# Kernel tuning notes

Hardware: AMD Instinct MI355X
Metric: run time of the kernel (lower is better)

Reference implementation:

```python
import jax, jax.numpy as jnp
import numpy as np

N, E, KS, DIM = 6890, 41340, 5, 2
K = KS * KS  # 25 spline kernel buckets


def spline_conv(x, edge_index, pseudo, weight, root, bias):
    """Degree-1 open B-spline conv (SplineGCN), mean aggregation + root + bias.
    x: [N, Fin], weight: [K, Fin, Fout], root: [Fin, Fout], bias: [Fout]."""
    row, col = edge_index[0], edge_index[1]  # target, source
    pos = pseudo * (KS - 1)                   # [E, 2] in [0, KS-1]
    i0 = jnp.clip(jnp.floor(pos), 0, KS - 2).astype(jnp.int32)  # [E, 2]
    frac = pos - i0                           # [E, 2]
    # 4 nonzero basis products per edge (2 per dim)
    off = jnp.array([[0, 0], [1, 0], [0, 1], [1, 1]], dtype=jnp.int32)  # [4, 2]
    b_dim = jnp.stack([1.0 - frac, frac], axis=-1)  # [E, 2, 2] (dim, which-knot)
    w = b_dim[:, 0, off[:, 0]] * b_dim[:, 1, off[:, 1]]       # [E, 4]
    idx = (i0[:, None, 0] + off[None, :, 0]) + KS * (i0[:, None, 1] + off[None, :, 1])  # [E, 4]
    # transform all nodes by all K kernels once: [N, K, Fout]
    xw = jnp.einsum('ni,kio->nko', x, weight)
    g = xw[col[:, None], idx]                 # [E, 4, Fout] gather
    msg = jnp.einsum('es,eso->eo', w, g)      # [E, Fout]
    agg = jax.ops.segment_sum(msg, row, num_segments=N)
    deg = jax.ops.segment_sum(jnp.ones((E,), x.dtype), row, num_segments=N)
    agg = agg / jnp.maximum(deg, 1.0)[:, None]
    return agg + x @ root + bias


def setup_inputs() -> dict:
    key = jax.random.key(0)
    ks = jax.random.split(key, 20)
    def gl(k, shape):  # glorot-ish
        fan = shape[-2] if len(shape) > 1 else shape[-1]
        return jax.random.normal(k, shape, jnp.float32) / np.sqrt(fan)
    inp = {
        'x': jax.random.normal(ks[0], (N, 544), jnp.float32),
        'edge_index': jax.random.randint(ks[1], (2, E), 0, N),
        'pseudo': jax.random.uniform(ks[2], (E, DIM), jnp.float32),
        'W_lin': gl(ks[3], (544, 16)), 'b_lin': jnp.zeros((16,), jnp.float32),
        'w1': gl(ks[4], (K, 16, 32)),  'r1': gl(ks[5], (16, 32)),  'bi1': jnp.zeros((32,), jnp.float32),
        'w2': gl(ks[6], (K, 32, 64)),  'r2': gl(ks[7], (32, 64)),  'bi2': jnp.zeros((64,), jnp.float32),
        'w3': gl(ks[8], (K, 64, 128)), 'r3': gl(ks[9], (64, 128)), 'bi3': jnp.zeros((128,), jnp.float32),
        'W1': gl(ks[10], (128, 256)), 'b1': jnp.zeros((256,), jnp.float32),
        'W2': gl(ks[11], (256, 6890)), 'b2': jnp.zeros((6890,), jnp.float32),
    }
    return inp


def reference(x, edge_index, pseudo, W_lin, b_lin, w1, r1, bi1, w2, r2, bi2, w3, r3, bi3, W1, b1, W2, b2):
    h = jax.nn.elu(x @ W_lin + b_lin)
    h = jax.nn.elu(spline_conv(h, edge_index, pseudo, w1, r1, bi1))
    h = jax.nn.elu(spline_conv(h, edge_index, pseudo, w2, r2, bi2))
    h = jax.nn.elu(spline_conv(h, edge_index, pseudo, w3, r3, bi3))
    h = jax.nn.elu(h @ W1 + b1)
    # dropout is identity in eval mode
    logits = h @ W2 + b2
    return jax.nn.log_softmax(logits, axis=-1)
```

## Files before the change

### kernel.cpp

```cpp
#include <hip/hip_runtime.h>
#include <hip/hip_bf16.h>

#define NND 6890
#define NED 41340

typedef __bf16 bf16x8 __attribute__((ext_vector_type(8)));
typedef float f32x4 __attribute__((ext_vector_type(4)));
typedef unsigned short u16x4 __attribute__((ext_vector_type(4)));

__device__ inline unsigned short f32_bf16(float f) {
  unsigned int u = __float_as_uint(f);
  unsigned int r = (u + 0x7FFFu + ((u >> 16) & 1u)) >> 16;
  return (unsigned short)r;
}
__device__ inline void split2(float v, unsigned short& hi, unsigned short& lo) {
  unsigned short h = f32_bf16(v);
  float hf = __uint_as_float((unsigned int)h << 16);
  hi = h;
  lo = f32_bf16(v - hf);
}
__device__ inline float elu_f(float v) { return v > 0.f ? v : (expf(v) - 1.f); }

__device__ __forceinline__ void gload_lds16(const void* g, void* l) {
  __builtin_amdgcn_global_load_lds((const __attribute__((address_space(1))) void*)g,
                                   (__attribute__((address_space(3))) void*)l, 16, 0, 0);
}

__global__ void edge_prep_kernel(const int* __restrict__ erow, const float* __restrict__ pseudo,
                                 float* __restrict__ ew, int* __restrict__ ek,
                                 int* __restrict__ deg, int E) {
  int e = blockIdx.x * blockDim.x + threadIdx.x;
  if (e >= E) return;
  float p0 = pseudo[2 * e + 0] * 4.0f;
  float p1 = pseudo[2 * e + 1] * 4.0f;
  int i0 = (int)floorf(p0); i0 = i0 < 0 ? 0 : (i0 > 3 ? 3 : i0);
  int i1 = (int)floorf(p1); i1 = i1 < 0 ? 0 : (i1 > 3 ? 3 : i1);
  float f0 = p0 - (float)i0, f1 = p1 - (float)i1;
  ew[4 * e + 0] = (1.f - f0) * (1.f - f1);
  ew[4 * e + 1] = f0 * (1.f - f1);
  ew[4 * e + 2] = (1.f - f0) * f1;
  ew[4 * e + 3] = f0 * f1;
  int b = i0 + 5 * i1;
  ek[4 * e + 0] = b; ek[4 * e + 1] = b + 1; ek[4 * e + 2] = b + 5; ek[4 * e + 3] = b + 6;
  atomicAdd(&deg[erow[e]], 1);
}

__global__ void scan_kernel(const int* __restrict__ deg, int* __restrict__ rowptr,
                            int* __restrict__ cursor, float* __restrict__ deginv, int n) {
  __shared__ int part[1024];
  int t = threadIdx.x;
  int CH = (n + 1023) >> 10;
  int base = t * CH;
  int s = 0;
  for (int j = 0; j < CH; ++j) { int i = base + j; if (i < n) s += deg[i]; }
  part[t] = s;
  __syncthreads();
  for (int off = 1; off < 1024; off <<= 1) {
    int v = (t >= off) ? part[t - off] : 0;
    __syncthreads();
    part[t] += v;
    __syncthreads();
  }
  int run = (t == 0) ? 0 : part[t - 1];
  for (int j = 0; j < CH; ++j) {
    int i = base + j;
    if (i < n) {
      rowptr[i] = run; cursor[i] = run;
      int d = deg[i];
      deginv[i] = 1.0f / fmaxf((float)d, 1.0f);
      run += d;
    }
  }
  if (t == 1023) rowptr[n] = part[1023];
}

__global__ void csr_fill_kernel(const int* __restrict__ erow, int* __restrict__ cursor,
                                int* __restrict__ csr, int E) {
  int e = blockIdx.x * blockDim.x + threadIdx.x;
  if (e >= E) return;
  int slot = atomicAdd(&cursor[erow[e]], 1);
  csr[slot] = e;
}

__global__ void prep_all_kernel(const float* __restrict__ W_lin, const float* __restrict__ w1,
                                const float* __restrict__ r1, const float* __restrict__ w2,
                                const float* __restrict__ r2, const float* __restrict__ w3,
                                const float* __restrict__ r3, const float* __restrict__ W1,
                                const float* __restrict__ x, const float* __restrict__ W2,
                                unsigned short* __restrict__ Th, unsigned short* __restrict__ Tl,
                                unsigned short* __restrict__ xh, unsigned short* __restrict__ xl,
                                unsigned short* __restrict__ W2t) {
  int b = blockIdx.x;
  int tid = threadIdx.x;
  if (b < 323) {
    const int tstart[9] = {0, 17, 30, 31, 81, 83, 283, 291, 323};
    const int jK[8]    = {544, 400, 16, 800, 32, 1600, 64, 128};
    const int jF[8]    = {16, 32, 32, 64, 64, 128, 128, 256};
    const int jldt[8]  = {544, 416, 416, 832, 832, 1664, 1664, 128};
    const int jkoff[8] = {0, 0, 400, 0, 800, 0, 1600, 0};
    const int jdst[8]  = {0, 8704, 8704, 22016, 22016, 75264, 75264, 288256};
    int job = 0;
    while (job < 7 && b >= tstart[job + 1]) ++job;
    int t = b - tstart[job];
    int fxc = (jF[job] + 31) >> 5;
    int kt = t / fxc, ft = t % fxc;
    const float* src;
    switch (job) {
      case 0: src = W_lin; break;
      case 1: src = w1; break;
      case 2: src = r1; break;
      case 3: src = w2; break;
      case 4: src = r2; break;
      case 5: src = w3; break;
      case 6: src = r3; break;
      default: src = W1; break;
    }
    int K = jK[job], F = jF[job], ldt = jldt[job], koff = jkoff[job];
    unsigned short* th = Th + jdst[job];
    unsigned short* tl = Tl + jdst[job];
    int k0 = kt * 32, c0 = ft * 32;
    __shared__ float tbuf[32][33];
    int tx = tid & 31, ty = tid >> 5;
    for (int j = ty; j < 32; j += 8) {
      int gk = k0 + j, gc = c0 + tx;
      tbuf[j][tx] = (gk < K && gc < F) ? src[(size_t)gk * F + gc] : 0.f;
    }
    __syncthreads();
    for (int j = ty; j < 32; j += 8) {
      int gc = c0 + j, gk = k0 + tx;
      if (gc < F && gk < K) {
        unsigned short h, lo2;
        split2(tbuf[tx][j], h, lo2);
        th[(size_t)gc * ldt + koff + gk] = h;
        tl[(size_t)gc * ldt + koff + gk] = lo2;
      }
    }
  } else if (b < 3984) {
    int i = (b - 323) * 256 + tid;
    if (i < NND * 136) {
      f32x4 v = *(const f32x4*)(x + 4 * (size_t)i);
      u16x4 h, l;
#pragma unroll
      for (int j = 0; j < 4; ++j) {
        unsigned short hh, ll;
        split2(v[j], hh, ll);
        h[j] = hh; l[j] = ll;
      }
      *(u16x4*)(xh + 4 * (size_t)i) = h;
      *(u16x4*)(xl + 4 * (size_t)i) = l;
    }
  } else {
    int t = b - 3984;
    int c0 = (t % 216) * 32, k0 = (t / 216) * 32;
    __shared__ float tb2[32][33];
    int tx = tid & 31, ty = tid >> 5;
    for (int j = ty; j < 32; j += 8) {
      int gk = k0 + j, gc = c0 + tx;
      tb2[j][tx] = (gk < 256 && gc < NND) ? W2[(size_t)gk * NND + gc] : 0.f;
    }
    __syncthreads();
    for (int j = ty; j < 32; j += 8) {
      int gc = c0 + j, gk = k0 + tx;
      if (gc < NND && gk < 256) W2t[(size_t)gc * 256 + gk] = f32_bf16(tb2[tx][j]);
    }
  }
}

__global__ void b_build_kernel(const float* __restrict__ x, const int* __restrict__ ecol,
                               const float* __restrict__ ew4, const int* __restrict__ ek4,
                               const int* __restrict__ rowptr, const int* __restrict__ csr,
                               const float* __restrict__ deginv,
                               unsigned short* __restrict__ Bh, unsigned short* __restrict__ Bl,
                               int Fin) {
  extern __shared__ float lds[];
  int r = blockIdx.x;
  int T = blockDim.x;
  int tid = threadIdx.x;
  int nb = 25 * Fin;
  int j = tid / Fin;
  int i = tid - j * Fin;
  float* plane = lds + j * nb;
  for (int t = tid; t < 4 * nb; t += T) lds[t] = 0.f;
  __syncthreads();
  int p0 = rowptr[r], p1 = rowptr[r + 1];
  for (int p = p0 + j; p < p1; p += 4) {
    int e = csr[p];
    int c = ecol[e];
    float xv = x[(size_t)c * Fin + i];
    f32x4 wv = *(const f32x4*)(ew4 + 4 * e);
    int4 kv = *(const int4*)(ek4 + 4 * e);
    plane[kv.x * Fin + i] += wv[0] * xv;
    plane[kv.y * Fin + i] += wv[1] * xv;
    plane[kv.z * Fin + i] += wv[2] * xv;
    plane[kv.w * Fin + i] += wv[3] * xv;
  }
  __syncthreads();
  float dinv = deginv[r];
  int tot = nb + Fin;
  for (int t = tid; t < tot; t += T) {
    float v;
    if (t < nb)
      v = (lds[t] + lds[nb + t] + lds[2 * nb + t] + lds[3 * nb + t]) * dinv;
    else
      v = x[(size_t)r * Fin + (t - nb)];
    unsigned short h, l;
    split2(v, h, l);
    Bh[(size_t)r * tot + t] = h;
    Bl[(size_t)r * tot + t] = l;
  }
}

template <int BN>
__global__ __launch_bounds__(256) void gemm_x3_partial_kernel(
    const unsigned short* __restrict__ Ah, const unsigned short* __restrict__ Al,
    const unsigned short* __restrict__ Wh, const unsigned short* __restrict__ Wl,
    float* __restrict__ P, int M, int Kd, int F, int KS) {
  constexpr int AE = 64 * 32;
  constexpr int WE = BN * 32;
  __shared__ __align__(16) unsigned short lds[2][2 * AE + 2 * WE];
  int tid = threadIdx.x;
  int wave = tid >> 6, lane = tid & 63;
  int g = lane >> 4, r = lane & 15;
  int row0 = blockIdx.y * 64;
  int col0 = blockIdx.x * BN;
  int z = blockIdx.z;
  int nt = Kd >> 5;
  int ta = z * nt / KS, tb = (z + 1) * nt / KS;

  auto STAGE = [&](int buf, int kb) {
    {
      int rr = tid >> 2, pos = tid & 3;
      int c = (pos - rr) & 3;
      int gra = row0 + rr; if (gra >= M) gra = M - 1;
      size_t so = (size_t)gra * Kd + kb + c * 8;
      gload_lds16(Ah + so, &lds[buf][wave * 512]);
      gload_lds16(Al + so, &lds[buf][AE + wave * 512]);
    }
#pragma unroll
    for (int it = 0; it < (4 * BN + 255) / 256; ++it) {
      int idx = it * 256 + tid;
      if (idx < 4 * BN) {
        int rr = idx >> 2, pos = idx & 3;
        int c = (pos - rr) & 3;
        size_t so = (size_t)(col0 + rr) * Kd + kb + c * 8;
        gload_lds16(Wh + so, &lds[buf][2 * AE + (it * 256 + wave * 64) * 8]);
        gload_lds16(Wl + so, &lds[buf][2 * AE + WE + (it * 256 + wave * 64) * 8]);
      }
    }
  };

  constexpr int NF = BN / 16;
  f32x4 acc[NF];
#pragma unroll
  for (int n = 0; n < NF; ++n)
#pragma unroll
    for (int q = 0; q < 4; ++q) acc[n][q] = 0.f;

  int n = tb - ta;
  int rA = wave * 16 + r;
  int aoff = rA * 32 + ((g + rA) & 3) * 8;

  STAGE(0, ta * 32);
  __syncthreads();
  for (int tt = 0; tt < n; ++tt) {
    int buf = tt & 1;
    if (tt + 1 < n) STAGE(buf ^ 1, (ta + tt + 1) * 32);
    bf16x8 fah = *(const bf16x8*)&lds[buf][aoff];
    bf16x8 fal = *(const bf16x8*)&lds[buf][AE + aoff];
#pragma unroll
    for (int nn = 0; nn < NF; ++nn) {
      int rW = nn * 16 + r;
      int woff = rW * 32 + ((g + rW) & 3) * 8;
      bf16x8 fbh = *(const bf16x8*)&lds[buf][2 * AE + woff];
      bf16x8 fbl = *(const bf16x8*)&lds[buf][2 * AE + WE + woff];
      acc[nn] = __builtin_amdgcn_mfma_f32_16x16x32_bf16(fah, fbh, acc[nn], 0, 0, 0);
      acc[nn] = __builtin_amdgcn_mfma_f32_16x16x32_bf16(fal, fbh, acc[nn], 0, 0, 0);
      acc[nn] = __builtin_amdgcn_mfma_f32_16x16x32_bf16(fah, fbl, acc[nn], 0, 0, 0);
    }
    __syncthreads();
  }
#pragma unroll
  for (int nn = 0; nn < NF; ++nn) {
    int gc = col0 + nn * 16 + r;
#pragma unroll
    for (int q = 0; q < 4; ++q) {
      int gr = row0 + wave * 16 + g * 4 + q;
      if (gr < M) P[((size_t)z * M + gr) * F + gc] = acc[nn][q];
    }
  }
}

__global__ __launch_bounds__(256) void combine_elu_kernel(
    const float* __restrict__ P, const float* __restrict__ bias,
    float* __restrict__ outF, unsigned short* __restrict__ outB,
    unsigned short* __restrict__ outH, unsigned short* __restrict__ outL,
    int M, int F, int KS) {
  int i4 = blockIdx.x * 256 + threadIdx.x;
  int fv = F >> 2;
  int total = M * fv;
  if (i4 >= total) return;
  int gr = i4 / fv, c4 = (i4 - gr * fv) * 4;
  f32x4 s = {0.f, 0.f, 0.f, 0.f};
  for (int z = 0; z < KS; ++z)
    s += *(const f32x4*)(P + ((size_t)z * M + gr) * F + c4);
  f32x4 bv = *(const f32x4*)(bias + c4);
#pragma unroll
  for (int j = 0; j < 4; ++j) s[j] = elu_f(s[j] + bv[j]);
  if (outH) {
    u16x4 h, l;
#pragma unroll
    for (int j = 0; j < 4; ++j) {
      unsigned short hh, ll;
      split2(s[j], hh, ll);
      h[j] = hh; l[j] = ll;
    }
    *(u16x4*)(outH + (size_t)gr * F + c4) = h;
    *(u16x4*)(outL + (size_t)gr * F + c4) = l;
  } else if (outB) {
    u16x4 o;
#pragma unroll
    for (int j = 0; j < 4; ++j) o[j] = f32_bf16(s[j]);
    *(u16x4*)(outB + (size_t)gr * F + c4) = o;
  } else {
    *(f32x4*)(outF + (size_t)gr * F + c4) = s;
  }
}

template <int MODE>
__global__ __launch_bounds__(256) void gemm_final_kernel(
    const unsigned short* __restrict__ A, const unsigned short* __restrict__ Bt,
    const float* __restrict__ bias, const float* __restrict__ lse,
    float* __restrict__ outp, int M, int N) {
  __shared__ __align__(16) unsigned short lds[2][2][4096];
  int tid = threadIdx.x;
  int w = tid >> 6, l = tid & 63;
  int row0 = blockIdx.y * 128, col0 = blockIdx.x * 128;

  auto STAGE = [&](int buf, int kb) {
#pragma unroll
    for (int it = 0; it < 2; ++it) {
      int idx = it * 256 + tid;
      int rr = idx >> 2, pos = idx & 3;
      int c = (pos - rr) & 3;
      int gra = row0 + rr; if (gra >= M) gra = M - 1;
      int grb = col0 + rr; if (grb >= N) grb = N - 1;
      gload_lds16(A + (size_t)gra * 256 + kb + c * 8, &lds[buf][0][(it * 256 + w * 64) * 8]);
      gload_lds16(Bt + (size_t)grb * 256 + kb + c * 8, &lds[buf][1][(it * 256 + w * 64) * 8]);
    }
  };

  int wm = w >> 1, wn = w & 1;
  int g = l >> 4, r = l & 15;

  f32x4 acc[4][4];
#pragma unroll
  for (int mi = 0; mi < 4; ++mi)
#pragma unroll
    for (int ni = 0; ni < 4; ++ni)
#pragma unroll
      for (int q = 0; q < 4; ++q) acc[mi][ni][q] = 0.f;

  STAGE(0, 0);
  __syncthreads();
#pragma unroll
  for (int ks = 0; ks < 8; ++ks) {
    int buf = ks & 1;
    if (ks < 7) STAGE(buf ^ 1, (ks + 1) * 32);
    bf16x8 fa[4], fb[4];
#pragma unroll
    for (int mi = 0; mi < 4; ++mi) {
      int rA = wm * 64 + mi * 16 + r;
      fa[mi] = *(const bf16x8*)&lds[buf][0][rA * 32 + ((g + rA) & 3) * 8];
    }
#pragma unroll
    for (int ni = 0; ni < 4; ++ni) {
      int rB = wn * 64 + ni * 16 + r;
      fb[ni] = *(const bf16x8*)&lds[buf][1][rB * 32 + ((g + rB) & 3) * 8];
    }
#pragma unroll
    for (int mi = 0; mi < 4; ++mi)
#pragma unroll
      for (int ni = 0; ni < 4; ++ni)
        acc[mi][ni] = __builtin_amdgcn_mfma_f32_16x16x32_bf16(fb[ni], fa[mi], acc[mi][ni], 0, 0, 0);
    __syncthreads();
  }

  if (MODE == 0) {
    float bb[4][4];
#pragma unroll
    for (int ni = 0; ni < 4; ++ni) {
      int gc0 = col0 + wn * 64 + ni * 16 + g * 4;
#pragma unroll
      for (int q = 0; q < 4; ++q)
        bb[ni][q] = (gc0 + q < N) ? bias[gc0 + q] : 0.f;
    }
#pragma unroll
    for (int mi = 0; mi < 4; ++mi) {
      int gr = row0 + wm * 64 + mi * 16 + r;
      float vv[4][4];
      float mloc = -3e38f;
#pragma unroll
      for (int ni = 0; ni < 4; ++ni) {
        int gc0 = col0 + wn * 64 + ni * 16 + g * 4;
#pragma unroll
        for (int q = 0; q < 4; ++q) {
          float v = (gc0 + q < N) ? (acc[mi][ni][q] + bb[ni][q]) : -3e38f;
          vv[ni][q] = v;
          mloc = fmaxf(mloc, v);
        }
      }
      float sloc = 0.f;
#pragma unroll
      for (int ni = 0; ni < 4; ++ni) {
        int gc0 = col0 + wn * 64 + ni * 16 + g * 4;
#pragma unroll
        for (int q = 0; q < 4; ++q)
          if (gc0 + q < N) sloc += __expf(vv[ni][q] - mloc);
      }
#pragma unroll
      for (int off = 16; off < 64; off <<= 1) {
        float mo = __shfl_xor(mloc, off);
        float so = __shfl_xor(sloc, off);
        float mn = fmaxf(mloc, mo);
        sloc = sloc * __expf(mloc - mn) + so * __expf(mo - mn);
        mloc = mn;
      }
      if (g == 0 && gr < M) {
        int hb = blockIdx.x * 2 + wn;
        *(float2*)(outp + 2 * ((size_t)hb * M + gr)) = make_float2(mloc, sloc);
      }
    }
  } else {
    float* LBUF = (float*)&lds[0][0][0];
#pragma unroll
    for (int p = 0; p < 2; ++p) {
      __syncthreads();
#pragma unroll
      for (int mh = 0; mh < 2; ++mh) {
        int mi = 2 * p + mh;
        int lr = wm * 32 + mh * 16 + r;
#pragma unroll
        for (int ni = 0; ni < 4; ++ni) {
          int ch = wn * 16 + ni * 4 + g;
          int u = (ch + lr) & 31;
          *(f32x4*)(LBUF + lr * 128 + u * 4) = acc[mi][ni];
        }
      }
      __syncthreads();
#pragma unroll
      for (int t = 0; t < 8; ++t) {
        int unit = t * 256 + tid;
        int lr = unit >> 5, ch = unit & 31;
        int gr = row0 + (lr >> 5) * 64 + p * 32 + ((lr >> 4) & 1) * 16 + (lr & 15);
        if (gr >= M) continue;
        int u = (ch + lr) & 31;
        f32x4 v = *(const f32x4*)(LBUF + lr * 128 + u * 4);
        float L = lse[gr];
        int gc0 = col0 + ch * 4;
        if (gc0 + 4 <= N) {
          f32x4 bv = *(const f32x4*)(bias + gc0);
#pragma unroll
          for (int q = 0; q < 4; ++q) v[q] = v[q] + bv[q] - L;
          *(f32x4*)(outp + (size_t)gr * N + gc0) = v;
        } else {
#pragma unroll
          for (int q = 0; q < 4; ++q)
            if (gc0 + q < N) outp[(size_t)gr * N + gc0 + q] = v[q] + bias[gc0 + q] - L;
        }
      }
    }
  }
}

__global__ __launch_bounds__(256) void lse_kernel(const float* __restrict__ stats,
                                                  float* __restrict__ lse, int M, int NH) {
  int row = blockIdx.x * 256 + threadIdx.x;
  if (row >= M) return;
  float m = -3e38f, s = 0.f;
  for (int hb = 0; hb < NH; ++hb) {
    float2 v = *(const float2*)(stats + 2 * ((size_t)hb * M + row));
    float mn = fmaxf(m, v.x);
    s = s * __expf(m - mn) + v.y * __expf(v.x - mn);
    m = mn;
  }
  lse[row] = m + logf(s);
}

extern "C" void kernel_launch(void* const* d_in, const int* in_sizes, int n_in,
                              void* d_out, int out_size, void* d_ws, size_t ws_size,
                              hipStream_t stream) {
  const int N = NND, E = NED;
  const float* x      = (const float*)d_in[0];
  const int*   ei     = (const int*)d_in[1];
  const float* pseudo = (const float*)d_in[2];
  const float* W_lin  = (const float*)d_in[3];
  const float* b_lin  = (const float*)d_in[4];
  const float* w1  = (const float*)d_in[5];
  const float* r1  = (const float*)d_in[6];
  const float* bi1 = (const float*)d_in[7];
  const float* w2  = (const float*)d_in[8];
  const float* r2  = (const float*)d_in[9];
  const float* bi2 = (const float*)d_in[10];
  const float* w3  = (const float*)d_in[11];
  const float* r3  = (const float*)d_in[12];
  const float* bi3 = (const float*)d_in[13];
  const float* W1  = (const float*)d_in[14];
  const float* b1  = (const float*)d_in[15];
  const float* W2  = (const float*)d_in[16];
  const float* b2  = (const float*)d_in[17];
  const int* erow = ei;
  const int* ecol = ei + E;

  char* scratch = (char*)d_out;
  size_t off = 0;
  auto alloc = [&](size_t bytes) -> void* {
    void* p = scratch + off;
    off = (off + bytes + 255) & ~(size_t)255;
    return p;
  };
  unsigned short* Bh = (unsigned short*)alloc((size_t)N * 1664 * 2);
  unsigned short* Bl = (unsigned short*)alloc((size_t)N * 1664 * 2);
  float* h0     = (float*)alloc((size_t)N * 16 * 4);
  float* h1     = (float*)alloc((size_t)N * 32 * 4);
  float* h2     = (float*)alloc((size_t)N * 64 * 4);
  unsigned short* h3h = (unsigned short*)alloc((size_t)N * 128 * 2);
  unsigned short* h3l = (unsigned short*)alloc((size_t)N * 128 * 2);
  unsigned short* xh  = (unsigned short*)alloc((size_t)N * 544 * 2);
  unsigned short* xl  = (unsigned short*)alloc((size_t)N * 544 * 2);
  unsigned short* Wth = (unsigned short*)alloc((size_t)321024 * 2);
  unsigned short* Wtl = (unsigned short*)alloc((size_t)321024 * 2);
  float* Pbuf   = (float*)alloc((size_t)4 * N * 128 * 4);
  float* stats  = (float*)alloc((size_t)108 * N * 2 * 4);
  float* ew     = (float*)alloc((size_t)E * 4 * 4);
  int*   ek     = (int*)alloc((size_t)E * 4 * 4);
  int*   deg    = (int*)alloc((size_t)N * 4);
  float* deginv = (float*)alloc((size_t)N * 4);
  int*   rowptr = (int*)alloc((size_t)(N + 1) * 4);
  int*   cursor = (int*)alloc((size_t)N * 4);
  int*   csr    = (int*)alloc((size_t)E * 4);

  unsigned short* h4b = (unsigned short*)d_ws;
  unsigned short* W2t = (unsigned short*)((char*)d_ws + (size_t)N * 256 * 2);
  float* lse = (float*)((char*)d_ws + (size_t)N * 256 * 4);

  hipMemsetAsync(deg, 0, (size_t)N * 4, stream);
  edge_prep_kernel<<<(E + 255) / 256, 256, 0, stream>>>(erow, pseudo, ew, ek, deg, E);
  scan_kernel<<<1, 1024, 0, stream>>>(deg, rowptr, cursor, deginv, N);
  csr_fill_kernel<<<(E + 255) / 256, 256, 0, stream>>>(erow, cursor, csr, E);

  prep_all_kernel<<<5712, 256, 0, stream>>>(W_lin, w1, r1, w2, r2, w3, r3, W1, x, W2,
                                            Wth, Wtl, xh, xl, W2t);

  auto cgrid = [](int M_, int F_) { return dim3((M_ * (F_ / 4) + 255) / 256); };

  gemm_x3_partial_kernel<16><<<dim3(1, 108, 4), 256, 0, stream>>>(xh, xl, Wth + 0, Wtl + 0, Pbuf, N, 544, 16, 4);
  combine_elu_kernel<<<cgrid(N, 16), 256, 0, stream>>>(Pbuf, b_lin, h0, nullptr, nullptr, nullptr, N, 16, 4);

  b_build_kernel<<<N, 64, 4 * 25 * 16 * 4, stream>>>(h0, ecol, ew, ek, rowptr, csr, deginv, Bh, Bl, 16);
  gemm_x3_partial_kernel<32><<<dim3(1, 108, 4), 256, 0, stream>>>(Bh, Bl, Wth + 8704, Wtl + 8704, Pbuf, N, 416, 32, 4);
  combine_elu_kernel<<<cgrid(N, 32), 256, 0, stream>>>(Pbuf, bi1, h1, nullptr, nullptr, nullptr, N, 32, 4);

  b_build_kernel<<<N, 128, 4 * 25 * 32 * 4, stream>>>(h1, ecol, ew, ek, rowptr, csr, deginv, Bh, Bl, 32);
  gemm_x3_partial_kernel<64><<<dim3(1, 108, 4), 256, 0, stream>>>(Bh, Bl, Wth + 22016, Wtl + 22016, Pbuf, N, 832, 64, 4);
  combine_elu_kernel<<<cgrid(N, 64), 256, 0, stream>>>(Pbuf, bi2, h2, nullptr, nullptr, nullptr, N, 64, 4);

  b_build_kernel<<<N, 256, 4 * 25 * 64 * 4, stream>>>(h2, ecol, ew, ek, rowptr, csr, deginv, Bh, Bl, 64);
  gemm_x3_partial_kernel<128><<<dim3(1, 108, 4), 256, 0, stream>>>(Bh, Bl, Wth + 75264, Wtl + 75264, Pbuf, N, 1664, 128, 4);
  combine_elu_kernel<<<cgrid(N, 128), 256, 0, stream>>>(Pbuf, bi3, nullptr, nullptr, h3h, h3l, N, 128, 4);

  gemm_x3_partial_kernel<128><<<dim3(2, 108, 2), 256, 0, stream>>>(h3h, h3l, Wth + 288256, Wtl + 288256, Pbuf, N, 128, 256, 2);
  combine_elu_kernel<<<cgrid(N, 256), 256, 0, stream>>>(Pbuf, b1, nullptr, h4b, nullptr, nullptr, N, 256, 2);

  gemm_final_kernel<0><<<dim3(54, 54), 256, 0, stream>>>(h4b, W2t, b2, nullptr, stats, N, N);

  lse_kernel<<<(N + 255) / 256, 256, 0, stream>>>(stats, lse, N, 108);

  gemm_final_kernel<1><<<dim3(54, 54), 256, 0, stream>>>(h4b, W2t, b2, lse, (float*)d_out, N, N);

  (void)in_sizes; (void)n_in; (void)out_size; (void)ws_size;
}
```

Baseline: 306.3 us.

## Fuse combine+ELU into b_build, merge edge prep, remap final GEMM for XCDs

Edge preprocessing moves into the prep_all kernel as extra blocks, removing one launch. The three early combine_elu launches are dropped: b_build now sums the split-K partials and applies bias and ELU inline for each gathered neighbour, at the cost of redundant reads and exp per edge. The final GEMM uses a 1D grid with an XCD-aware block remapping to improve L2 locality. Separate partial buffers per layer replace the shared Pbuf.

```diff
diff --git a/kernel.cpp b/kernel.cpp
--- a/kernel.cpp
+++ b/kernel.cpp
@@ -21,28 +21,17 @@
 }
 __device__ inline float elu_f(float v) { return v > 0.f ? v : (expf(v) - 1.f); }
 
+__device__ __forceinline__ float prev_h(const float* __restrict__ P,
+                                        const float* __restrict__ bias,
+                                        int Fin, int KS, int c, int i) {
+  float s = 0.f;
+  for (int z = 0; z < KS; ++z) s += P[((size_t)z * NND + c) * Fin + i];
+  return elu_f(s + bias[i]);
+}
+
 __device__ __forceinline__ void gload_lds16(const void* g, void* l) {
   __builtin_amdgcn_global_load_lds((const __attribute__((address_space(1))) void*)g,
                                    (__attribute__((address_space(3))) void*)l, 16, 0, 0);
-}
-
-__global__ void edge_prep_kernel(const int* __restrict__ erow, const float* __restrict__ pseudo,
-                                 float* __restrict__ ew, int* __restrict__ ek,
-                                 int* __restrict__ deg, int E) {
-  int e = blockIdx.x * blockDim.x + threadIdx.x;
-  if (e >= E) return;
-  float p0 = pseudo[2 * e + 0] * 4.0f;
-  float p1 = pseudo[2 * e + 1] * 4.0f;
-  int i0 = (int)floorf(p0); i0 = i0 < 0 ? 0 : (i0 > 3 ? 3 : i0);
-  int i1 = (int)floorf(p1); i1 = i1 < 0 ? 0 : (i1 > 3 ? 3 : i1);
-  float f0 = p0 - (float)i0, f1 = p1 - (float)i1;
-  ew[4 * e + 0] = (1.f - f0) * (1.f - f1);
-  ew[4 * e + 1] = f0 * (1.f - f1);
-  ew[4 * e + 2] = (1.f - f0) * f1;
-  ew[4 * e + 3] = f0 * f1;
-  int b = i0 + 5 * i1;
-  ek[4 * e + 0] = b; ek[4 * e + 1] = b + 1; ek[4 * e + 2] = b + 5; ek[4 * e + 3] = b + 6;
-  atomicAdd(&deg[erow[e]], 1);
 }
 
 __global__ void scan_kernel(const int* __restrict__ deg, int* __restrict__ rowptr,
@@ -87,9 +76,12 @@
                                 const float* __restrict__ r2, const float* __restrict__ w3,
                                 const float* __restrict__ r3, const float* __restrict__ W1,
                                 const float* __restrict__ x, const float* __restrict__ W2,
+                                const int* __restrict__ erow, const float* __restrict__ pseudo,
                                 unsigned short* __restrict__ Th, unsigned short* __restrict__ Tl,
                                 unsigned short* __restrict__ xh, unsigned short* __restrict__ xl,
-                                unsigned short* __restrict__ W2t) {
+                                unsigned short* __restrict__ W2t,
+                                float* __restrict__ ew, int* __restrict__ ek,
+                                int* __restrict__ deg) {
   int b = blockIdx.x;
   int tid = threadIdx.x;
   if (b < 323) {
@@ -149,7 +141,7 @@
       *(u16x4*)(xh + 4 * (size_t)i) = h;
       *(u16x4*)(xl + 4 * (size_t)i) = l;
     }
-  } else {
+  } else if (b < 5712) {
     int t = b - 3984;
     int c0 = (t % 216) * 32, k0 = (t / 216) * 32;
     __shared__ float tb2[32][33];
@@ -163,15 +155,32 @@
       int gc = c0 + j, gk = k0 + tx;
       if (gc < NND && gk < 256) W2t[(size_t)gc * 256 + gk] = f32_bf16(tb2[tx][j]);
     }
-  }
-}
-
-__global__ void b_build_kernel(const float* __restrict__ x, const int* __restrict__ ecol,
+  } else {
+    int e = (b - 5712) * 256 + tid;
+    if (e < NED) {
+      float p0 = pseudo[2 * e + 0] * 4.0f;
+      float p1 = pseudo[2 * e + 1] * 4.0f;
+      int i0 = (int)floorf(p0); i0 = i0 < 0 ? 0 : (i0 > 3 ? 3 : i0);
+      int i1 = (int)floorf(p1); i1 = i1 < 0 ? 0 : (i1 > 3 ? 3 : i1);
+      float f0 = p0 - (float)i0, f1 = p1 - (float)i1;
+      ew[4 * e + 0] = (1.f - f0) * (1.f - f1);
+      ew[4 * e + 1] = f0 * (1.f - f1);
+      ew[4 * e + 2] = (1.f - f0) * f1;
+      ew[4 * e + 3] = f0 * f1;
+      int bb = i0 + 5 * i1;
+      ek[4 * e + 0] = bb; ek[4 * e + 1] = bb + 1; ek[4 * e + 2] = bb + 5; ek[4 * e + 3] = bb + 6;
+      atomicAdd(&deg[erow[e]], 1);
+    }
+  }
+}
+
+__global__ void b_build_kernel(const float* __restrict__ P, const float* __restrict__ bias,
+                               const int* __restrict__ ecol,
                                const float* __restrict__ ew4, const int* __restrict__ ek4,
                                const int* __restrict__ rowptr, const int* __restrict__ csr,
                                const float* __restrict__ deginv,
                                unsigned short* __restrict__ Bh, unsigned short* __restrict__ Bl,
-                               int Fin) {
+                               int Fin, int KS) {
   extern __shared__ float lds[];
   int r = blockIdx.x;
   int T = blockDim.x;
@@ -186,7 +195,7 @@
   for (int p = p0 + j; p < p1; p += 4) {
     int e = csr[p];
     int c = ecol[e];
-    float xv = x[(size_t)c * Fin + i];
+    float xv = prev_h(P, bias, Fin, KS, c, i);
     f32x4 wv = *(const f32x4*)(ew4 + 4 * e);
     int4 kv = *(const int4*)(ek4 + 4 * e);
     plane[kv.x * Fin + i] += wv[0] * xv;
@@ -202,7 +211,7 @@
     if (t < nb)
       v = (lds[t] + lds[nb + t] + lds[2 * nb + t] + lds[3 * nb + t]) * dinv;
     else
-      v = x[(size_t)r * Fin + (t - nb)];
+      v = prev_h(P, bias, Fin, KS, r, t - nb);
     unsigned short h, l;
     split2(v, h, l);
     Bh[(size_t)r * tot + t] = h;
@@ -292,7 +301,7 @@
 
 __global__ __launch_bounds__(256) void combine_elu_kernel(
     const float* __restrict__ P, const float* __restrict__ bias,
-    float* __restrict__ outF, unsigned short* __restrict__ outB,
+    unsigned short* __restrict__ outB,
     unsigned short* __restrict__ outH, unsigned short* __restrict__ outL,
     int M, int F, int KS) {
   int i4 = blockIdx.x * 256 + threadIdx.x;
@@ -316,13 +325,11 @@
     }
     *(u16x4*)(outH + (size_t)gr * F + c4) = h;
     *(u16x4*)(outL + (size_t)gr * F + c4) = l;
-  } else if (outB) {
+  } else {
     u16x4 o;
 #pragma unroll
     for (int j = 0; j < 4; ++j) o[j] = f32_bf16(s[j]);
     *(u16x4*)(outB + (size_t)gr * F + c4) = o;
-  } else {
-    *(f32x4*)(outF + (size_t)gr * F + c4) = s;
   }
 }
 
@@ -334,7 +341,13 @@
   __shared__ __align__(16) unsigned short lds[2][2][4096];
   int tid = threadIdx.x;
   int w = tid >> 6, l = tid & 63;
-  int row0 = blockIdx.y * 128, col0 = blockIdx.x * 128;
+  int orig = blockIdx.x;
+  const int nwg = 54 * 54, q = nwg >> 3, r8 = nwg & 7;
+  int xcd = orig & 7, k = orig >> 3;
+  int base = (xcd < r8) ? xcd * (q + 1) : r8 * (q + 1) + (xcd - r8) * q;
+  int wg = base + k;
+  int by = wg / 54, bx = wg - by * 54;
+  int row0 = by * 128, col0 = bx * 128;
 
   auto STAGE = [&](int buf, int kb) {
 #pragma unroll
@@ -358,7 +371,7 @@
 #pragma unroll
     for (int ni = 0; ni < 4; ++ni)
 #pragma unroll
-      for (int q = 0; q < 4; ++q) acc[mi][ni][q] = 0.f;
+      for (int q2 = 0; q2 < 4; ++q2) acc[mi][ni][q2] = 0.f;
 
   STAGE(0, 0);
   __syncthreads();
@@ -391,8 +404,8 @@
     for (int ni = 0; ni < 4; ++ni) {
       int gc0 = col0 + wn * 64 + ni * 16 + g * 4;
 #pragma unroll
-      for (int q = 0; q < 4; ++q)
-        bb[ni][q] = (gc0 + q < N) ? bias[gc0 + q] : 0.f;
+      for (int q2 = 0; q2 < 4; ++q2)
+        bb[ni][q2] = (gc0 + q2 < N) ? bias[gc0 + q2] : 0.f;
     }
 #pragma unroll
     for (int mi = 0; mi < 4; ++mi) {
@@ -403,9 +416,9 @@
       for (int ni = 0; ni < 4; ++ni) {
         int gc0 = col0 + wn * 64 + ni * 16 + g * 4;
 #pragma unroll
-        for (int q = 0; q < 4; ++q) {
-          float v = (gc0 + q < N) ? (acc[mi][ni][q] + bb[ni][q]) : -3e38f;
-          vv[ni][q] = v;
+        for (int q2 = 0; q2 < 4; ++q2) {
+          float v = (gc0 + q2 < N) ? (acc[mi][ni][q2] + bb[ni][q2]) : -3e38f;
+          vv[ni][q2] = v;
           mloc = fmaxf(mloc, v);
         }
       }
@@ -414,8 +427,8 @@
       for (int ni = 0; ni < 4; ++ni) {
         int gc0 = col0 + wn * 64 + ni * 16 + g * 4;
 #pragma unroll
-        for (int q = 0; q < 4; ++q)
-          if (gc0 + q < N) sloc += __expf(vv[ni][q] - mloc);
+        for (int q2 = 0; q2 < 4; ++q2)
+          if (gc0 + q2 < N) sloc += __expf(vv[ni][q2] - mloc);
       }
 #pragma unroll
       for (int off = 16; off < 64; off <<= 1) {
@@ -426,7 +439,7 @@
         mloc = mn;
       }
       if (g == 0 && gr < M) {
-        int hb = blockIdx.x * 2 + wn;
+        int hb = bx * 2 + wn;
         *(float2*)(outp + 2 * ((size_t)hb * M + gr)) = make_float2(mloc, sloc);
       }
     }
@@ -460,12 +473,12 @@
         if (gc0 + 4 <= N) {
           f32x4 bv = *(const f32x4*)(bias + gc0);
 #pragma unroll
-          for (int q = 0; q < 4; ++q) v[q] = v[q] + bv[q] - L;
+          for (int q2 = 0; q2 < 4; ++q2) v[q2] = v[q2] + bv[q2] - L;
           *(f32x4*)(outp + (size_t)gr * N + gc0) = v;
         } else {
 #pragma unroll
-          for (int q = 0; q < 4; ++q)
-            if (gc0 + q < N) outp[(size_t)gr * N + gc0 + q] = v[q] + bias[gc0 + q] - L;
+          for (int q2 = 0; q2 < 4; ++q2)
+            if (gc0 + q2 < N) outp[(size_t)gr * N + gc0 + q2] = v[q2] + bias[gc0 + q2] - L;
         }
       }
     }
@@ -520,16 +533,17 @@
   };
   unsigned short* Bh = (unsigned short*)alloc((size_t)N * 1664 * 2);
   unsigned short* Bl = (unsigned short*)alloc((size_t)N * 1664 * 2);
-  float* h0     = (float*)alloc((size_t)N * 16 * 4);
-  float* h1     = (float*)alloc((size_t)N * 32 * 4);
-  float* h2     = (float*)alloc((size_t)N * 64 * 4);
   unsigned short* h3h = (unsigned short*)alloc((size_t)N * 128 * 2);
   unsigned short* h3l = (unsigned short*)alloc((size_t)N * 128 * 2);
   unsigned short* xh  = (unsigned short*)alloc((size_t)N * 544 * 2);
   unsigned short* xl  = (unsigned short*)alloc((size_t)N * 544 * 2);
   unsigned short* Wth = (unsigned short*)alloc((size_t)321024 * 2);
   unsigned short* Wtl = (unsigned short*)alloc((size_t)321024 * 2);
-  float* Pbuf   = (float*)alloc((size_t)4 * N * 128 * 4);
+  float* P0 = (float*)alloc((size_t)4 * N * 16 * 4);
+  float* P1 = (float*)alloc((size_t)4 * N * 32 * 4);
+  float* P2 = (float*)alloc((size_t)4 * N * 64 * 4);
+  float* P3 = (float*)alloc((size_t)4 * N * 128 * 4);
+  float* P4 = (float*)alloc((size_t)2 * N * 256 * 4);
   float* stats  = (float*)alloc((size_t)108 * N * 2 * 4);
   float* ew     = (float*)alloc((size_t)E * 4 * 4);
   int*   ek     = (int*)alloc((size_t)E * 4 * 4);
@@ -544,38 +558,31 @@
   float* lse = (float*)((char*)d_ws + (size_t)N * 256 * 4);
 
   hipMemsetAsync(deg, 0, (size_t)N * 4, stream);
-  edge_prep_kernel<<<(E + 255) / 256, 256, 0, stream>>>(erow, pseudo, ew, ek, deg, E);
+  prep_all_kernel<<<5874, 256, 0, stream>>>(W_lin, w1, r1, w2, r2, w3, r3, W1, x, W2,
+                                            erow, pseudo, Wth, Wtl, xh, xl, W2t, ew, ek, deg);
   scan_kernel<<<1, 1024, 0, stream>>>(deg, rowptr, cursor, deginv, N);
   csr_fill_kernel<<<(E + 255) / 256, 256, 0, stream>>>(erow, cursor, csr, E);
 
-  prep_all_kernel<<<5712, 256, 0, stream>>>(W_lin, w1, r1, w2, r2, w3, r3, W1, x, W2,
-                                            Wth, Wtl, xh, xl, W2t);
-
-  auto cgrid = [](int M_, int F_) { return dim3((M_ * (F_ / 4) + 255) / 256); };
-
-  gemm_x3_partial_kernel<16><<<dim3(1, 108, 4), 256, 0, stream>>>(xh, xl, Wth + 0, Wtl + 0, Pbuf, N, 544, 16, 4);
-  combine_elu_kernel<<<cgrid(N, 16), 256, 0, stream>>>(Pbuf, b_lin, h0, nullptr, nullptr, nullptr, N, 16, 4);
-
-  b_build_kernel<<<N, 64, 4 * 25 * 16 * 4, stream>>>(h0, ecol, ew, ek, rowptr, csr, deginv, Bh, Bl, 16);
-  gemm_x3_partial_kernel<32><<<dim3(1, 108, 4), 256, 0, stream>>>(Bh, Bl, Wth + 8704, Wtl + 8704, Pbuf, N, 416, 32, 4);
-  combine_elu_kernel<<<cgrid(N, 32), 256, 0, stream>>>(Pbuf, bi1, h1, nullptr, nullptr, nullptr, N, 32, 4);
-
-  b_build_kernel<<<N, 128, 4 * 25 * 32 * 4, stream>>>(h1, ecol, ew, ek, rowptr, csr, deginv, Bh, Bl, 32);
-  gemm_x3_partial_kernel<64><<<dim3(1, 108, 4), 256, 0, stream>>>(Bh, Bl, Wth + 22016, Wtl + 22016, Pbuf, N, 832, 64, 4);
-  combine_elu_kernel<<<cgrid(N, 64), 256, 0, stream>>>(Pbuf, bi2, h2, nullptr, nullptr, nullptr, N, 64, 4);
-
-  b_build_kernel<<<N, 256, 4 * 25 * 64 * 4, stream>>>(h2, ecol, ew, ek, rowptr, csr, deginv, Bh, Bl, 64);
-  gemm_x3_partial_kernel<128><<<dim3(1, 108, 4), 256, 0, stream>>>(Bh, Bl, Wth + 75264, Wtl + 75264, Pbuf, N, 1664, 128, 4);
-  combine_elu_kernel<<<cgrid(N, 128), 256, 0, stream>>>(Pbuf, bi3, nullptr, nullptr, h3h, h3l, N, 128, 4);
-
-  gemm_x3_partial_kernel<128><<<dim3(2, 108, 2), 256, 0, stream>>>(h3h, h3l, Wth + 288256, Wtl + 288256, Pbuf, N, 128, 256, 2);
-  combine_elu_kernel<<<cgrid(N, 256), 256, 0, stream>>>(Pbuf, b1, nullptr, h4b, nullptr, nullptr, N, 256, 2);
-
-  gemm_final_kernel<0><<<dim3(54, 54), 256, 0, stream>>>(h4b, W2t, b2, nullptr, stats, N, N);
+  gemm_x3_partial_kernel<16><<<dim3(1, 108, 4), 256, 0, stream>>>(xh, xl, Wth + 0, Wtl + 0, P0, N, 544, 16, 4);
+
+  b_build_kernel<<<N, 64, 4 * 25 * 16 * 4, stream>>>(P0, b_lin, ecol, ew, ek, rowptr, csr, deginv, Bh, Bl, 16, 4);
+  gemm_x3_partial_kernel<32><<<dim3(1, 108, 4), 256, 0, stream>>>(Bh, Bl, Wth + 8704, Wtl + 8704, P1, N, 416, 32, 4);
+
+  b_build_kernel<<<N, 128, 4 * 25 * 32 * 4, stream>>>(P1, bi1, ecol, ew, ek, rowptr, csr, deginv, Bh, Bl, 32, 4);
+  gemm_x3_partial_kernel<64><<<dim3(1, 108, 4), 256, 0, stream>>>(Bh, Bl, Wth + 22016, Wtl + 22016, P2, N, 832, 64, 4);
+
+  b_build_kernel<<<N, 256, 4 * 25 * 64 * 4, stream>>>(P2, bi2, ecol, ew, ek, rowptr, csr, deginv, Bh, Bl, 64, 4);
+  gemm_x3_partial_kernel<128><<<dim3(1, 108, 4), 256, 0, stream>>>(Bh, Bl, Wth + 75264, Wtl + 75264, P3, N, 1664, 128, 4);
+  combine_elu_kernel<<<(N * 32 + 255) / 256, 256, 0, stream>>>(P3, bi3, nullptr, h3h, h3l, N, 128, 4);
+
+  gemm_x3_partial_kernel<128><<<dim3(2, 108, 2), 256, 0, stream>>>(h3h, h3l, Wth + 288256, Wtl + 288256, P4, N, 128, 256, 2);
+  combine_elu_kernel<<<(N * 64 + 255) / 256, 256, 0, stream>>>(P4, b1, h4b, nullptr, nullptr, N, 256, 2);
+
+  gemm_final_kernel<0><<<dim3(54 * 54), 256, 0, stream>>>(h4b, W2t, b2, nullptr, stats, N, N);
 
   lse_kernel<<<(N + 255) / 256, 256, 0, stream>>>(stats, lse, N, 108);
 
-  gemm_final_kernel<1><<<dim3(54, 54), 256, 0, stream>>>(h4b, W2t, b2, lse, (float*)d_out, N, N);
+  gemm_final_kernel<1><<<dim3(54 * 54), 256, 0, stream>>>(h4b, W2t, b2, lse, (float*)d_out, N, N);
 
   (void)in_sizes; (void)n_in; (void)out_size; (void)ws_size;
 }
```

New measurement: 320.3 us. 1.05x slower.
